# Kernel tuning notes

Measured on AMD Instinct MI355X. Metric: run time of the kernel, lower is better.

The kernel has to match this reference:

```python
import jax, jax.numpy as jnp
import numpy as np

N = 50000      # nodes
E = 800000     # edges (before self-loops)
IN_DIM = 128
HID = 96
PROJ = 64
BN_EPS = 1e-5
L2_EPS = 1e-12


def setup_inputs() -> dict:
    key = jax.random.key(0)
    ks = jax.random.split(key, 8)

    def glorot(k, shape):
        fan_in, fan_out = shape
        s = np.sqrt(6.0 / (fan_in + fan_out)).astype(np.float32)
        return jax.random.uniform(k, shape, jnp.float32, -s, s)

    x = jax.random.normal(ks[0], (N, IN_DIM), jnp.float32)
    edge_index = jax.random.randint(ks[1], (2, E), 0, N, dtype=jnp.int64)

    return {
        "x": x,
        "edge_index": edge_index,
        # GCN layer 1
        "W1": glorot(ks[2], (IN_DIM, HID)), "b1": jnp.zeros(HID, jnp.float32),
        "g1": jnp.ones(HID, jnp.float32), "be1": jnp.zeros(HID, jnp.float32),
        # GCN layer 2
        "W2": glorot(ks[3], (HID, HID)), "b2": jnp.zeros(HID, jnp.float32),
        "g2": jnp.ones(HID, jnp.float32), "be2": jnp.zeros(HID, jnp.float32),
        # projector: Linear -> BN -> ReLU -> Linear
        "Wp1": glorot(ks[4], (HID, HID)), "bp1": jnp.zeros(HID, jnp.float32),
        "gp": jnp.ones(HID, jnp.float32), "bep": jnp.zeros(HID, jnp.float32),
        "Wp2": glorot(ks[5], (HID, PROJ)), "bp2": jnp.zeros(PROJ, jnp.float32),
    }


def _batchnorm(h, gamma, beta):
    # training-mode BatchNorm1d: batch stats, biased variance
    m = h.mean(axis=0)
    v = h.var(axis=0)
    return gamma * (h - m) * jax.lax.rsqrt(v + BN_EPS) + beta


def _gcn_conv(x, W, b, src, dst, deg_inv_sqrt):
    # PyG GCNConv: x @ W, symmetric-normalized scatter-add (self-loops included
    # in src/dst), then bias.
    xw = x @ W                                              # [N, out]
    norm = deg_inv_sqrt[src] * deg_inv_sqrt[dst]            # [E+N]
    msg = xw[src] * norm[:, None]                           # [E+N, out]
    out = jax.ops.segment_sum(msg, dst, num_segments=x.shape[0])
    return out + b


def reference(x, edge_index, W1, b1, g1, be1, W2, b2, g2, be2,
              Wp1, bp1, gp, bep, Wp2, bp2):
    n = x.shape[0]
    loops = jnp.arange(n, dtype=edge_index.dtype)
    src = jnp.concatenate([edge_index[0], loops])
    dst = jnp.concatenate([edge_index[1], loops])
    deg = jax.ops.segment_sum(jnp.ones(src.shape[0], x.dtype), dst,
                              num_segments=n)               # includes self-loops
    deg_inv_sqrt = jax.lax.rsqrt(deg)                       # deg >= 1 always

    h = jax.nn.relu(_batchnorm(_gcn_conv(x, W1, b1, src, dst, deg_inv_sqrt), g1, be1))
    h = jax.nn.relu(_batchnorm(_gcn_conv(h, W2, b2, src, dst, deg_inv_sqrt), g2, be2))

    z = jax.nn.relu(_batchnorm(h @ Wp1 + bp1, gp, bep))
    z = z @ Wp2 + bp2
    # F.normalize(p=2, dim=-1, eps=1e-12)
    nrm = jnp.linalg.norm(z, axis=-1, keepdims=True)
    return z / jnp.maximum(nrm, L2_EPS)
```

## Files before the change

### kernel.cpp

```cpp
#include <hip/hip_runtime.h>
#include <hip/hip_fp16.h>

constexpr int BLK = 256;

static inline int cdiv(long long a, int b) { return (int)((a + b - 1) / b); }

using v8h = __attribute__((ext_vector_type(8))) _Float16;
using v4f = __attribute__((ext_vector_type(4))) float;



__global__ __launch_bounds__(256) void scan1_dis(const int* __restrict__ cnt,
                                                 int* __restrict__ rowptr,
                                                 int* __restrict__ bsum,
                                                 float* __restrict__ dis, int N) {
    __shared__ int ts[256];
    int tid = threadIdx.x;
    int base = blockIdx.x * 1024 + tid * 4;
    int v[4], s = 0;
#pragma unroll
    for (int i = 0; i < 4; ++i) {
        v[i] = (base + i < N) ? cnt[base + i] : 0;
        s += v[i];
        if (base + i < N) dis[base + i] = rsqrtf((float)v[i] + 1.0f);
    }
    ts[tid] = s;
    __syncthreads();
    for (int off = 1; off < 256; off <<= 1) {
        int t = 0;
        if (tid >= off) t = ts[tid - off];
        __syncthreads();
        if (tid >= off) ts[tid] += t;
        __syncthreads();
    }
    int run = ts[tid] - s;
#pragma unroll
    for (int i = 0; i < 4; ++i) {
        if (base + i < N) rowptr[base + i] = run;
        run += v[i];
    }
    if (tid == 255) bsum[blockIdx.x] = ts[255];
}

__global__ __launch_bounds__(256) void scan23(int* __restrict__ rowptr,
                                              const int* __restrict__ bsum,
                                              int nb, int N, int E) {
    __shared__ int sboff[64];
    const int tid = threadIdx.x;
    if (tid < 64) {
        int orig = (tid < nb) ? bsum[tid] : 0;
        int v = orig;
#pragma unroll
        for (int off = 1; off < 64; off <<= 1) {
            int t = __shfl_up(v, off, 64);
            if (tid >= off) v += t;
        }
        sboff[tid] = v - orig;
    }
    __syncthreads();
    int i = blockIdx.x * 256 + tid;
    if (i < N) rowptr[i] += sboff[i >> 10];
    if (i == 0) rowptr[N] = E;
}

__global__ void csr_fill(const int* __restrict__ src, const int* __restrict__ dst,
                         const unsigned short* __restrict__ eoff,
                         const int* __restrict__ rowptr,
                         unsigned short* __restrict__ csrc, int E) {
    for (int i = blockIdx.x * blockDim.x + threadIdx.x; i < E; i += gridDim.x * blockDim.x) {
        csrc[rowptr[dst[i]] + (int)eoff[i]] = (unsigned short)src[i];
    }
}


template <int K, bool ACT, bool BIAS, bool STATS, bool OUTSP, typename TIN>
__device__ __forceinline__ void gemm96_body(int bid,
                                            const TIN* __restrict__ in,
                                            const float* __restrict__ W,
                                            const float* __restrict__ bias,
                                            const float* __restrict__ bnsums,
                                            const float* __restrict__ gamma,
                                            const float* __restrict__ beta,
                                            const float* __restrict__ dsc,
                                            _Float16* __restrict__ hout,
                                            float* __restrict__ osums, int N) {
    constexpr int NK = K / 32;
    constexpr int LDK = K + 8;
    __shared__ __align__(16) _Float16 Wt[96 * LDK];
    __shared__ __align__(16) float ssl[ACT ? 192 : 1];
    __shared__ float sb[STATS ? 192 : 1];
    const int tid = threadIdx.x;
    for (int idx = tid; idx < K * 96; idx += 256) {
        int k = idx / 96, n = idx - k * 96;
        Wt[n * LDK + k] = (_Float16)W[idx];
    }
    if (ACT && tid < 96) {
        float inv_n = 1.0f / (float)N;
        float mean = bnsums[tid] * inv_n;
        float var = bnsums[96 + tid] * inv_n - mean * mean;
        float sc = gamma[tid] * rsqrtf(var + 1e-5f);
        ssl[tid] = sc;
        ssl[96 + tid] = beta[tid] - mean * sc;
    }
    if (STATS && tid < 192) sb[tid] = 0.0f;
    __syncthreads();

    const int wave = tid >> 6, lane = tid & 63;
    const int quad = lane >> 4, lm = lane & 15;
    const int rbase = bid * 64 + wave * 16;
    int arow = rbase + lm;
    arow = arow < N ? arow : N - 1;

    v8h afr[NK];
#pragma unroll
    for (int kc = 0; kc < NK; ++kc) {
        const int kk = kc * 32 + quad * 8;
        if constexpr (sizeof(TIN) == 4) {
            const float* p = (const float*)&in[(long long)arow * K + kk];
            float4 p0 = *(const float4*)p;
            float4 p1 = *(const float4*)(p + 4);
            if (ACT) {
                float4 sc0 = *(const float4*)&ssl[kk];
                float4 sc1 = *(const float4*)&ssl[kk + 4];
                float4 sh0 = *(const float4*)&ssl[96 + kk];
                float4 sh1 = *(const float4*)&ssl[96 + kk + 4];
                p0.x = fmaxf(fmaf(p0.x, sc0.x, sh0.x), 0.0f);
                p0.y = fmaxf(fmaf(p0.y, sc0.y, sh0.y), 0.0f);
                p0.z = fmaxf(fmaf(p0.z, sc0.z, sh0.z), 0.0f);
                p0.w = fmaxf(fmaf(p0.w, sc0.w, sh0.w), 0.0f);
                p1.x = fmaxf(fmaf(p1.x, sc1.x, sh1.x), 0.0f);
                p1.y = fmaxf(fmaf(p1.y, sc1.y, sh1.y), 0.0f);
                p1.z = fmaxf(fmaf(p1.z, sc1.z, sh1.z), 0.0f);
                p1.w = fmaxf(fmaf(p1.w, sc1.w, sh1.w), 0.0f);
            }
            v8h a;
            a[0] = (_Float16)p0.x; a[1] = (_Float16)p0.y;
            a[2] = (_Float16)p0.z; a[3] = (_Float16)p0.w;
            a[4] = (_Float16)p1.x; a[5] = (_Float16)p1.y;
            a[6] = (_Float16)p1.z; a[7] = (_Float16)p1.w;
            afr[kc] = a;
        } else {
            v8h hv = *(const v8h*)&in[(long long)arow * 96 + kk];
            if (ACT) {
#pragma unroll
                for (int j = 0; j < 8; ++j) {
                    float f = (float)hv[j];
                    f = fmaxf(fmaf(f, ssl[kk + j], ssl[96 + kk + j]), 0.0f);
                    hv[j] = (_Float16)f;
                }
            }
            afr[kc] = hv;
        }
    }

    v4f acc[6];
#pragma unroll
    for (int t = 0; t < 6; ++t) {
        v4f c = {0.0f, 0.0f, 0.0f, 0.0f};
#pragma unroll
        for (int kc = 0; kc < NK; ++kc) {
            v8h b = *(const v8h*)&Wt[(t * 16 + lm) * LDK + kc * 32 + quad * 8];
            c = __builtin_amdgcn_mfma_f32_16x16x32_f16(afr[kc], b, c, 0, 0, 0);
        }
        acc[t] = c;
    }

    float dr[4];
#pragma unroll
    for (int r = 0; r < 4; ++r) {
        int gr = rbase + quad * 4 + r;
        dr[r] = dsc ? dsc[gr < N ? gr : N - 1] : 1.0f;
    }

    float ls[6], lq[6];
#pragma unroll
    for (int t = 0; t < 6; ++t) { ls[t] = 0.0f; lq[t] = 0.0f; }
#pragma unroll
    for (int t = 0; t < 6; ++t) {
        float bv = BIAS ? bias[t * 16 + lm] : 0.0f;
#pragma unroll
        for (int r = 0; r < 4; ++r) {
            int gr = rbase + quad * 4 + r;
            if (gr < N) {
                float o = acc[t][r] + bv;
                if (OUTSP) {
                    hout[(((long long)(t >> 1) * N + gr) * 32) + (t & 1) * 16 + lm] =
                        (_Float16)(o * dr[r]);
                } else {
                    hout[(long long)gr * 96 + t * 16 + lm] = (_Float16)(o * dr[r]);
                }
                if (STATS) { ls[t] += o; lq[t] += o * o; }
            }
        }
    }
    if (STATS) {
#pragma unroll
        for (int t = 0; t < 6; ++t) {
            ls[t] += __shfl_xor(ls[t], 16);
            ls[t] += __shfl_xor(ls[t], 32);
            lq[t] += __shfl_xor(lq[t], 16);
            lq[t] += __shfl_xor(lq[t], 32);
        }
        if (quad == 0) {
#pragma unroll
            for (int t = 0; t < 6; ++t) {
                atomicAdd(&sb[t * 16 + lm], ls[t]);
                atomicAdd(&sb[96 + t * 16 + lm], lq[t]);
            }
        }
        __syncthreads();
        if (tid < 192) atomicAdd(&osums[tid], sb[tid]);
    }
}

template <int K, bool ACT, bool BIAS, bool STATS, bool OUTSP, typename TIN>
__global__ __launch_bounds__(256) void gemm96m(const TIN* __restrict__ in,
                                               const float* __restrict__ W,
                                               const float* __restrict__ bias,
                                               const float* __restrict__ bnsums,
                                               const float* __restrict__ gamma,
                                               const float* __restrict__ beta,
                                               const float* __restrict__ dsc,
                                               _Float16* __restrict__ hout,
                                               float* __restrict__ osums, int N) {
    gemm96_body<K, ACT, BIAS, STATS, OUTSP, TIN>(blockIdx.x, in, W, bias, bnsums,
                                                 gamma, beta, dsc, hout, osums, N);
}

__global__ __launch_bounds__(256) void gemm1_count(const float* __restrict__ x,
                                                   const float* __restrict__ W1,
                                                   _Float16* __restrict__ hout,
                                                   const int* __restrict__ dst,
                                                   int* __restrict__ cnt,
                                                   unsigned short* __restrict__ eoff,
                                                   int gG, int N, int E) {
    if ((int)blockIdx.x < gG) {
        gemm96_body<128, false, false, false, true, float>(
            blockIdx.x, x, W1, nullptr, nullptr, nullptr, nullptr, nullptr,
            hout, nullptr, N);
    } else {
        int g = (blockIdx.x - gG) * 256 + threadIdx.x;
        int stride = (gridDim.x - gG) * 256;
        for (int i = g; i < E; i += stride)
            eoff[i] = (unsigned short)atomicAdd(&cnt[dst[i]], 1);
    }
}


__global__ __launch_bounds__(256) void gemm_finalm(const _Float16* __restrict__ in,
                                                   const float* __restrict__ W,
                                                   const float* __restrict__ bias,
                                                   const float* __restrict__ bnsums,
                                                   const float* __restrict__ gamma,
                                                   const float* __restrict__ beta,
                                                   float* __restrict__ out, int N) {
    constexpr int K = 96, NK = 3, LDK = K + 8;
    __shared__ __align__(16) _Float16 Wt[64 * LDK];
    __shared__ __align__(16) float ssl[192];
    const int tid = threadIdx.x;
    for (int idx = tid; idx < K * 64; idx += 256) {
        int k = idx / 64, n = idx - k * 64;
        Wt[n * LDK + k] = (_Float16)W[idx];
    }
    if (tid < 96) {
        float inv_n = 1.0f / (float)N;
        float mean = bnsums[tid] * inv_n;
        float var = bnsums[96 + tid] * inv_n - mean * mean;
        float sc = gamma[tid] * rsqrtf(var + 1e-5f);
        ssl[tid] = sc;
        ssl[96 + tid] = beta[tid] - mean * sc;
    }
    __syncthreads();

    const int wave = tid >> 6, lane = tid & 63;
    const int quad = lane >> 4, lm = lane & 15;
    const int rbase = blockIdx.x * 64 + wave * 16;
    int arow = rbase + lm;
    arow = arow < N ? arow : N - 1;

    v8h afr[NK];
#pragma unroll
    for (int kc = 0; kc < NK; ++kc) {
        const int kk = kc * 32 + quad * 8;
        v8h hv = *(const v8h*)&in[(long long)arow * 96 + kk];
#pragma unroll
        for (int j = 0; j < 8; ++j) {
            float f = (float)hv[j];
            f = fmaxf(fmaf(f, ssl[kk + j], ssl[96 + kk + j]), 0.0f);
            hv[j] = (_Float16)f;
        }
        afr[kc] = hv;
    }

    v4f acc[4];
#pragma unroll
    for (int t = 0; t < 4; ++t) {
        v4f c = {0.0f, 0.0f, 0.0f, 0.0f};
#pragma unroll
        for (int kc = 0; kc < NK; ++kc) {
            v8h b = *(const v8h*)&Wt[(t * 16 + lm) * LDK + kc * 32 + quad * 8];
            c = __builtin_amdgcn_mfma_f32_16x16x32_f16(afr[kc], b, c, 0, 0, 0);
        }
        float bv = bias[t * 16 + lm];
        c[0] += bv; c[1] += bv; c[2] += bv; c[3] += bv;
        acc[t] = c;
    }

    float sq[4];
#pragma unroll
    for (int r = 0; r < 4; ++r) {
        float s = acc[0][r] * acc[0][r] + acc[1][r] * acc[1][r] +
                  acc[2][r] * acc[2][r] + acc[3][r] * acc[3][r];
#pragma unroll
        for (int m = 1; m < 16; m <<= 1) s += __shfl_xor(s, m, 64);
        sq[r] = 1.0f / fmaxf(sqrtf(s), 1e-12f);
    }
#pragma unroll
    for (int r = 0; r < 4; ++r) {
        int gr = rbase + quad * 4 + r;
        if (gr < N) {
#pragma unroll
            for (int t = 0; t < 4; ++t)
                out[(long long)gr * 64 + t * 16 + lm] = acc[t][r] * sq[r];
        }
    }
}


template <bool PRESC>
__global__ __launch_bounds__(256) void agg32p(const __half* __restrict__ hxw,
                                              const int* __restrict__ rowptr,
                                              const unsigned short* __restrict__ csrc,
                                              const float* __restrict__ dis,
                                              const float* __restrict__ bias,
                                              _Float16* __restrict__ outh,
                                              int nchp, int N) {
    int nwg = gridDim.x;
    int wid = (blockIdx.x & 7) * (nwg >> 3) + (blockIdx.x >> 3);
    int plane = wid / nchp, chunk = wid - plane * nchp;
    int colth = threadIdx.x & 3;
    int n = chunk * 64 + (threadIdx.x >> 2);
    if (n >= N) return;
    const __half* hp = hxw + (long long)plane * N * 32 + colth * 8;
    float dn = dis[n];
    float acc[8];
    {
        float sw = PRESC ? 1.0f : dn;
        float4 g = *(const float4*)&hp[n * 32];
        const __half2* hs = (const __half2*)&g;
#pragma unroll
        for (int k = 0; k < 4; ++k) {
            float2 f = __half22float2(hs[k]);
            acc[2 * k + 0] = f.x * sw;
            acc[2 * k + 1] = f.y * sw;
        }
    }
    int e = rowptr[n], e1 = rowptr[n + 1];
    for (; e + 7 < e1; e += 8) {
        int s[8];
        float4 g[8];
        float w[8];
#pragma unroll
        for (int j = 0; j < 8; ++j) s[j] = csrc[e + j];
        if (!PRESC) {
#pragma unroll
            for (int j = 0; j < 8; ++j) w[j] = dis[s[j]];
        }
#pragma unroll
        for (int j = 0; j < 8; ++j) g[j] = *(const float4*)&hp[s[j] * 32];
#pragma unroll
        for (int j = 0; j < 8; ++j) {
            const __half2* h = (const __half2*)&g[j];
#pragma unroll
            for (int k = 0; k < 4; ++k) {
                float2 f = __half22float2(h[k]);
                if (PRESC) { acc[2 * k] += f.x; acc[2 * k + 1] += f.y; }
                else {
                    acc[2 * k]     = fmaf(f.x, w[j], acc[2 * k]);
                    acc[2 * k + 1] = fmaf(f.y, w[j], acc[2 * k + 1]);
                }
            }
        }
    }
    for (; e + 3 < e1; e += 4) {
        int s[4];
        float4 g[4];
        float w[4];
#pragma unroll
        for (int j = 0; j < 4; ++j) s[j] = csrc[e + j];
        if (!PRESC) {
#pragma unroll
            for (int j = 0; j < 4; ++j) w[j] = dis[s[j]];
        }
#pragma unroll
        for (int j = 0; j < 4; ++j) g[j] = *(const float4*)&hp[s[j] * 32];
#pragma unroll
        for (int j = 0; j < 4; ++j) {
            const __half2* h = (const __half2*)&g[j];
#pragma unroll
            for (int k = 0; k < 4; ++k) {
                float2 f = __half22float2(h[k]);
                if (PRESC) { acc[2 * k] += f.x; acc[2 * k + 1] += f.y; }
                else {
                    acc[2 * k]     = fmaf(f.x, w[j], acc[2 * k]);
                    acc[2 * k + 1] = fmaf(f.y, w[j], acc[2 * k + 1]);
                }
            }
        }
    }
    for (; e < e1; ++e) {
        int s0 = csrc[e];
        float w0 = PRESC ? 1.0f : dis[s0];
        float4 g0 = *(const float4*)&hp[s0 * 32];
        const __half2* h = (const __half2*)&g0;
#pragma unroll
        for (int k = 0; k < 4; ++k) {
            float2 f = __half22float2(h[k]);
            acc[2 * k]     = fmaf(f.x, w0, acc[2 * k]);
            acc[2 * k + 1] = fmaf(f.y, w0, acc[2 * k + 1]);
        }
    }
    const int ch = plane * 32 + colth * 8;
    v8h o;
#pragma unroll
    for (int j = 0; j < 8; ++j)
        o[j] = (_Float16)fmaf(acc[j], dn, bias[ch + j]);
    *(v8h*)&outh[(long long)n * 96 + ch] = o;
}


__global__ __launch_bounds__(256) void bn_stats96h(const __half* __restrict__ h,
                                                   float* __restrict__ sums, int N) {
    __shared__ float sb[192];
    const int tid = threadIdx.x;
    if (tid < 192) sb[tid] = 0.0f;
    __syncthreads();
    int g = blockIdx.x * 256 + tid;
    int total = N * 12, stride = gridDim.x * 256;
    int c8 = g % 12;
    float s[8] = {0, 0, 0, 0, 0, 0, 0, 0};
    float q[8] = {0, 0, 0, 0, 0, 0, 0, 0};
    for (int i = g; i < total; i += stride) {
        int n = i / 12;
        float4 raw = *(const float4*)&h[n * 96 + 8 * c8];
        const __half2* hp = (const __half2*)&raw;
#pragma unroll
        for (int k = 0; k < 4; ++k) {
            float2 f = __half22float2(hp[k]);
            s[2 * k + 0] += f.x;
            s[2 * k + 1] += f.y;
            q[2 * k + 0] += f.x * f.x;
            q[2 * k + 1] += f.y * f.y;
        }
    }
#pragma unroll
    for (int j = 0; j < 8; ++j) {
        atomicAdd(&sb[8 * c8 + j], s[j]);
        atomicAdd(&sb[96 + 8 * c8 + j], q[j]);
    }
    __syncthreads();
    if (tid < 192) atomicAdd(&sums[tid], sb[tid]);
}


extern "C" void kernel_launch(void* const* d_in, const int* in_sizes, int n_in,
                              void* d_out, int out_size, void* d_ws, size_t ws_size,
                              hipStream_t stream) {
    const float* x   = (const float*)d_in[0];
    const int*   ei  = (const int*)d_in[1];
    const float* W1  = (const float*)d_in[2];
    const float* b1  = (const float*)d_in[3];
    const float* g1  = (const float*)d_in[4];
    const float* be1 = (const float*)d_in[5];
    const float* W2  = (const float*)d_in[6];
    const float* b2  = (const float*)d_in[7];
    const float* g2  = (const float*)d_in[8];
    const float* be2 = (const float*)d_in[9];
    const float* Wp1 = (const float*)d_in[10];
    const float* bp1 = (const float*)d_in[11];
    const float* gp  = (const float*)d_in[12];
    const float* bep = (const float*)d_in[13];
    const float* Wp2 = (const float*)d_in[14];
    const float* bp2 = (const float*)d_in[15];

    const int N = in_sizes[0] / 128;
    const int E = in_sizes[1] / 2;
    const int* src = ei;
    const int* dst = ei + E;

    char* w = (char*)d_ws;
    auto alloc = [&](size_t bytes) { char* p = w; w += (bytes + 15) & ~size_t(15); return p; };
    int*            cnt    = (int*)alloc((size_t)N * 4);
    float*          sums   = (float*)alloc(576 * 4);
    int*            rowptr = (int*)alloc((size_t)(N + 1) * 4);
    int*            bsum   = (int*)alloc(64 * 4);
    float*          dis    = (float*)alloc((size_t)N * 4);
    unsigned short* eoff   = (unsigned short*)alloc((size_t)E * 2);
    unsigned short* csrc   = (unsigned short*)alloc((size_t)E * 2);
    _Float16*       buf2h  = (_Float16*)alloc((size_t)N * 96 * 2);
    _Float16*       hbuf   = (_Float16*)alloc((size_t)N * 96 * 2);
    float* sums1 = sums, *sums2 = sums + 192, *sums3 = sums + 384;

    float* out = (float*)d_out;

    const int gE   = cdiv(E, BLK);
    const int gG   = cdiv(N, 64);
    const int gC   = 1024;
    const int nb   = cdiv(N, 1024);
    const int nchp = (cdiv(N, 64) + 7) & ~7;
    const int gAgg = 3 * nchp;

    size_t zlen = (size_t)((char*)sums - (char*)cnt) + 576 * 4;
    hipMemsetAsync(cnt, 0, zlen, stream);

    gemm1_count<<<gG + gC, 256, 0, stream>>>(x, W1, hbuf, dst, cnt, eoff, gG, N, E);
    scan1_dis<<<nb, 256, 0, stream>>>(cnt, rowptr, bsum, dis, N);
    scan23<<<cdiv(N, 256), 256, 0, stream>>>(rowptr, bsum, nb, N, E);
    csr_fill<<<gE, BLK, 0, stream>>>(src, dst, eoff, rowptr, csrc, E);

    agg32p<false><<<gAgg, 256, 0, stream>>>((const __half*)hbuf, rowptr, csrc, dis,
                                            b1, buf2h, nchp, N);
    bn_stats96h<<<510, 256, 0, stream>>>((const __half*)buf2h, sums1, N);

    gemm96m<96, true, false, false, true, _Float16><<<gG, 256, 0, stream>>>(
        buf2h, W2, nullptr, sums1, g1, be1, dis, hbuf, nullptr, N);
    agg32p<true><<<gAgg, 256, 0, stream>>>((const __half*)hbuf, rowptr, csrc, dis,
                                           b2, buf2h, nchp, N);
    bn_stats96h<<<510, 256, 0, stream>>>((const __half*)buf2h, sums2, N);

    gemm96m<96, true, true, true, false, _Float16><<<gG, 256, 0, stream>>>(
        buf2h, Wp1, bp1, sums2, g2, be2, nullptr, hbuf, sums3, N);

    gemm_finalm<<<gG, 256, 0, stream>>>(hbuf, Wp2, bp2, sums3, gp, bep, out, N);
}
```

Before: 311.4 us.

## Sort nodes by in-degree for aggregation load balance; split gemm1 and edge count

Builds a 64-bin histogram of node in-degrees during the scan, then computes a degree-bucketed permutation of node ids. The aggregation kernels process nodes in that permuted order so the 64 nodes handled by one workgroup have similar edge counts, reducing divergence and tail imbalance within waves. The fused gemm1+edge-count kernel is split back into two separate launches, which adds a launch and loses their overlap. Writes now scatter to permuted node rows, which may reduce write locality.

```diff
diff --git a/kernel.cpp b/kernel.cpp
--- a/kernel.cpp
+++ b/kernel.cpp
@@ -9,13 +9,22 @@
 using v4f = __attribute__((ext_vector_type(4))) float;
 
 
+
+__global__ void count_dst_off(const int* __restrict__ dst, int* __restrict__ cnt,
+                              unsigned short* __restrict__ eoff, int E) {
+    for (int i = blockIdx.x * blockDim.x + threadIdx.x; i < E; i += gridDim.x * blockDim.x)
+        eoff[i] = (unsigned short)atomicAdd(&cnt[dst[i]], 1);
+}
 
 __global__ __launch_bounds__(256) void scan1_dis(const int* __restrict__ cnt,
                                                  int* __restrict__ rowptr,
                                                  int* __restrict__ bsum,
-                                                 float* __restrict__ dis, int N) {
+                                                 float* __restrict__ dis,
+                                                 int* __restrict__ ghist, int N) {
     __shared__ int ts[256];
+    __shared__ int lh[64];
     int tid = threadIdx.x;
+    if (tid < 64) lh[tid] = 0;
     int base = blockIdx.x * 1024 + tid * 4;
     int v[4], s = 0;
 #pragma unroll
@@ -26,6 +35,10 @@
     }
     ts[tid] = s;
     __syncthreads();
+#pragma unroll
+    for (int i = 0; i < 4; ++i) {
+        if (base + i < N) atomicAdd(&lh[v[i] < 63 ? v[i] : 63], 1);
+    }
     for (int off = 1; off < 256; off <<= 1) {
         int t = 0;
         if (tid >= off) t = ts[tid - off];
@@ -40,12 +53,22 @@
         run += v[i];
     }
     if (tid == 255) bsum[blockIdx.x] = ts[255];
+    __syncthreads();
+    if (tid < 64) {
+        int c = lh[tid];
+        if (c) atomicAdd(&ghist[tid], c);
+    }
 }
 
 __global__ __launch_bounds__(256) void scan23(int* __restrict__ rowptr,
                                               const int* __restrict__ bsum,
+                                              const int* __restrict__ cnt,
+                                              const int* __restrict__ ghist,
+                                              int* __restrict__ gcur,
+                                              unsigned short* __restrict__ perm,
                                               int nb, int N, int E) {
     __shared__ int sboff[64];
+    __shared__ int gb[64];
     const int tid = threadIdx.x;
     if (tid < 64) {
         int orig = (tid < nb) ? bsum[tid] : 0;
@@ -56,10 +79,26 @@
             if (tid >= off) v += t;
         }
         sboff[tid] = v - orig;
+    } else if (tid < 128) {
+        int b = tid - 64;
+        int h = ghist[b];
+        int v = h;
+#pragma unroll
+        for (int off = 1; off < 64; off <<= 1) {
+            int t = __shfl_up(v, off, 64);
+            if (b >= off) v += t;
+        }
+        gb[b] = v - h;
     }
     __syncthreads();
     int i = blockIdx.x * 256 + tid;
-    if (i < N) rowptr[i] += sboff[i >> 10];
+    if (i < N) {
+        rowptr[i] += sboff[i >> 10];
+        int d = cnt[i];
+        d = d < 63 ? d : 63;
+        int slot = gb[d] + atomicAdd(&gcur[d], 1);
+        perm[slot] = (unsigned short)i;
+    }
     if (i == 0) rowptr[N] = E;
 }
 
@@ -227,25 +266,6 @@
                                                  gamma, beta, dsc, hout, osums, N);
 }
 
-__global__ __launch_bounds__(256) void gemm1_count(const float* __restrict__ x,
-                                                   const float* __restrict__ W1,
-                                                   _Float16* __restrict__ hout,
-                                                   const int* __restrict__ dst,
-                                                   int* __restrict__ cnt,
-                                                   unsigned short* __restrict__ eoff,
-                                                   int gG, int N, int E) {
-    if ((int)blockIdx.x < gG) {
-        gemm96_body<128, false, false, false, true, float>(
-            blockIdx.x, x, W1, nullptr, nullptr, nullptr, nullptr, nullptr,
-            hout, nullptr, N);
-    } else {
-        int g = (blockIdx.x - gG) * 256 + threadIdx.x;
-        int stride = (gridDim.x - gG) * 256;
-        for (int i = g; i < E; i += stride)
-            eoff[i] = (unsigned short)atomicAdd(&cnt[dst[i]], 1);
-    }
-}
-
 
 __global__ __launch_bounds__(256) void gemm_finalm(const _Float16* __restrict__ in,
                                                    const float* __restrict__ W,
@@ -333,14 +353,16 @@
                                               const unsigned short* __restrict__ csrc,
                                               const float* __restrict__ dis,
                                               const float* __restrict__ bias,
+                                              const unsigned short* __restrict__ perm,
                                               _Float16* __restrict__ outh,
                                               int nchp, int N) {
     int nwg = gridDim.x;
     int wid = (blockIdx.x & 7) * (nwg >> 3) + (blockIdx.x >> 3);
     int plane = wid / nchp, chunk = wid - plane * nchp;
     int colth = threadIdx.x & 3;
-    int n = chunk * 64 + (threadIdx.x >> 2);
-    if (n >= N) return;
+    int slot = chunk * 64 + (threadIdx.x >> 2);
+    if (slot >= N) return;
+    int n = perm[slot];
     const __half* hp = hxw + (long long)plane * N * 32 + colth * 8;
     float dn = dis[n];
     float acc[8];
@@ -492,11 +514,14 @@
     auto alloc = [&](size_t bytes) { char* p = w; w += (bytes + 15) & ~size_t(15); return p; };
     int*            cnt    = (int*)alloc((size_t)N * 4);
     float*          sums   = (float*)alloc(576 * 4);
+    int*            ghist  = (int*)alloc(64 * 4);
+    int*            gcur   = (int*)alloc(64 * 4);
     int*            rowptr = (int*)alloc((size_t)(N + 1) * 4);
     int*            bsum   = (int*)alloc(64 * 4);
     float*          dis    = (float*)alloc((size_t)N * 4);
     unsigned short* eoff   = (unsigned short*)alloc((size_t)E * 2);
     unsigned short* csrc   = (unsigned short*)alloc((size_t)E * 2);
+    unsigned short* perm   = (unsigned short*)alloc((size_t)N * 2);
     _Float16*       buf2h  = (_Float16*)alloc((size_t)N * 96 * 2);
     _Float16*       hbuf   = (_Float16*)alloc((size_t)N * 96 * 2);
     float* sums1 = sums, *sums2 = sums + 192, *sums3 = sums + 384;
@@ -505,27 +530,29 @@
 
     const int gE   = cdiv(E, BLK);
     const int gG   = cdiv(N, 64);
-    const int gC   = 1024;
     const int nb   = cdiv(N, 1024);
     const int nchp = (cdiv(N, 64) + 7) & ~7;
     const int gAgg = 3 * nchp;
 
-    size_t zlen = (size_t)((char*)sums - (char*)cnt) + 576 * 4;
+    size_t zlen = (size_t)((char*)gcur - (char*)cnt) + 64 * 4;
     hipMemsetAsync(cnt, 0, zlen, stream);
 
-    gemm1_count<<<gG + gC, 256, 0, stream>>>(x, W1, hbuf, dst, cnt, eoff, gG, N, E);
-    scan1_dis<<<nb, 256, 0, stream>>>(cnt, rowptr, bsum, dis, N);
-    scan23<<<cdiv(N, 256), 256, 0, stream>>>(rowptr, bsum, nb, N, E);
+    gemm96m<128, false, false, false, true, float><<<gG, 256, 0, stream>>>(
+        x, W1, nullptr, nullptr, nullptr, nullptr, nullptr, hbuf, nullptr, N);
+    count_dst_off<<<gE, BLK, 0, stream>>>(dst, cnt, eoff, E);
+    scan1_dis<<<nb, 256, 0, stream>>>(cnt, rowptr, bsum, dis, ghist, N);
+    scan23<<<cdiv(N, 256), 256, 0, stream>>>(rowptr, bsum, cnt, ghist, gcur, perm,
+                                             nb, N, E);
     csr_fill<<<gE, BLK, 0, stream>>>(src, dst, eoff, rowptr, csrc, E);
 
     agg32p<false><<<gAgg, 256, 0, stream>>>((const __half*)hbuf, rowptr, csrc, dis,
-                                            b1, buf2h, nchp, N);
+                                            b1, perm, buf2h, nchp, N);
     bn_stats96h<<<510, 256, 0, stream>>>((const __half*)buf2h, sums1, N);
 
     gemm96m<96, true, false, false, true, _Float16><<<gG, 256, 0, stream>>>(
         buf2h, W2, nullptr, sums1, g1, be1, dis, hbuf, nullptr, N);
     agg32p<true><<<gAgg, 256, 0, stream>>>((const __half*)hbuf, rowptr, csrc, dis,
-                                           b2, buf2h, nchp, N);
+                                           b2, perm, buf2h, nchp, N);
     bn_stats96h<<<510, 256, 0, stream>>>((const __half*)buf2h, sums2, N);
 
     gemm96m<96, true, true, true, false, _Float16><<<gG, 256, 0, stream>>>(
```

New measurement: 446.5 us. 43.4% more time.
